# Performance work log

Measured on AMD Instinct MI355X. Metric: run time of the kernel, lower is better.

The kernel has to match this reference:

```python
import jax, jax.numpy as jnp
import numpy as np

S = 2048      # sequence length (q_seq == kv_seq, self-attention)
D = 1024      # hidden_size
H = 16        # num_heads
DH = D // H   # per-head dim
LN_EPS = 1e-5


def setup_inputs() -> dict:
    key = jax.random.key(0)
    ks = jax.random.split(key, 8)
    init = lambda k, shape: (jax.random.normal(k, shape, dtype=jnp.float32)
                             / np.float32(np.sqrt(shape[-1])))
    return {
        "x": jax.random.normal(ks[0], (S, D), dtype=jnp.float32),
        "logit_bias": jax.random.normal(ks[1], (S, H * S), dtype=jnp.float32) * 0.1,
        "mask": jax.random.bernoulli(ks[2], 0.9, (S, S)),
        "Wq": init(ks[3], (D, D)),
        "Wk": init(ks[4], (D, D)),
        "Wv": init(ks[5], (D, D)),
        "Wo": init(ks[6], (D, D)),
        "ln_w": jnp.ones((D,), dtype=jnp.float32),
        "ln_b": jnp.zeros((D,), dtype=jnp.float32),
    }


def reference(x, logit_bias, mask, Wq, Wk, Wv, Wo, ln_w, ln_b):
    # Projections (eqx.nn.Linear: y = W @ x, no bias), split into heads.
    q = (x @ Wq.T).reshape(S, H, DH)  # [s,h,d]
    k = (x @ Wk.T).reshape(S, H, DH)  # [S,h,d]
    v = (x @ Wv.T).reshape(S, H, DH)  # [S,h,d]

    # Scaled scores + per-head additive logit bias.
    scale = jnp.asarray(1.0 / np.sqrt(DH), dtype=q.dtype)
    logits = jnp.einsum('shd,Shd->hsS', q * scale, k)  # [h,s,S]
    logits = logits + logit_bias.reshape(S, H, S).transpose(1, 0, 2)

    # Boolean mask (q_seq, kv_seq) broadcast over heads.
    logits = jnp.where(mask[None, :, :], logits, jnp.finfo(logits.dtype).min)

    # Stable softmax in float32 (matches result_type promotion in source).
    weights = jax.nn.softmax(logits.astype(jnp.float32), axis=-1).astype(logits.dtype)

    attn = jnp.einsum('hsS,Shd->shd', weights, v).reshape(S, D)
    attn_out = attn @ Wo.T  # output projection, no bias

    # Residual + LayerNorm over last dim (eqx.nn.LayerNorm, eps=1e-5).
    res = attn_out + x
    mean = jnp.mean(res, axis=-1, keepdims=True)
    var = jnp.var(res, axis=-1, keepdims=True)
    normed = (res - mean) * jax.lax.rsqrt(var + LN_EPS)
    return normed * ln_w + ln_b
```

## Files before the change

kernel.cpp:

```cpp
#include <hip/hip_runtime.h>

#define SS 2048
#define DD 1024
#define HH 16
#define DHD 64
#define HSN (HH * SS)
#define LOG2E 1.44269504088896340736f

typedef __bf16 bf16x8 __attribute__((ext_vector_type(8)));
typedef __bf16 bf16x4 __attribute__((ext_vector_type(4)));
typedef float f32x4 __attribute__((ext_vector_type(4)));
typedef unsigned int u32;

__device__ __forceinline__ void glds16(const void* g, void* l) {
  __builtin_amdgcn_global_load_lds(
      (const __attribute__((address_space(1))) u32*)(const u32*)g,
      (__attribute__((address_space(3))) u32*)(u32*)l, 16, 0, 0);
}

__global__ __launch_bounds__(256) void cvt_all_kernel(const float* __restrict__ x,
                                                      const float* __restrict__ Wq,
                                                      const float* __restrict__ Wk,
                                                      const float* __restrict__ Wv,
                                                      const float* __restrict__ Wo,
                                                      __bf16* xb, __bf16* Wqb, __bf16* Wkb,
                                                      __bf16* Wvb, __bf16* Wob) {
  const int z = blockIdx.z;
  const int n4 = (z == 0 ? SS * DD : DD * DD) / 4;
  const int i = blockIdx.x * 256 + threadIdx.x;
  if (i >= n4) return;
  const float* in = z == 0 ? x : (z == 1 ? Wq : (z == 2 ? Wk : (z == 3 ? Wv : Wo)));
  __bf16* out = z == 0 ? xb : (z == 1 ? Wqb : (z == 2 ? Wkb : (z == 3 ? Wvb : Wob)));
  const float4 v = ((const float4*)in)[i];
  bf16x4 r;
  r[0] = (__bf16)v.x; r[1] = (__bf16)v.y; r[2] = (__bf16)v.z; r[3] = (__bf16)v.w;
  *(bf16x4*)&out[(long)i * 4] = r;
}

template <int OUTF32>
__device__ __forceinline__ void gemm128_body(const __bf16* __restrict__ A,
                                             const __bf16* __restrict__ B,
                                             void* __restrict__ Cout, float scale) {
  __shared__ alignas(16) __bf16 As[128 * 32];
  __shared__ alignas(16) __bf16 Bs[128 * 32];
  const int tid = threadIdx.x;
  const int lane = tid & 63;
  const int wave = tid >> 6;
  const long m0 = (long)blockIdx.y * 128;
  const long n0 = (long)blockIdx.x * 128;
  const int wm = (wave >> 1) * 64;
  const int wn = (wave & 1) * 64;
  const int g = lane >> 4, r16 = lane & 15;
  const int srow = tid >> 2, sseg = (tid & 3) * 8;

  f32x4 acc[4][4] = {};

  for (int k0 = 0; k0 < DD; k0 += 32) {
#pragma unroll
    for (int it = 0; it < 2; ++it) {
      const int row = srow + it * 64;
      glds16(&A[(m0 + row) * DD + k0 + sseg], &As[row * 32 + sseg]);
      glds16(&B[(n0 + row) * DD + k0 + sseg], &Bs[row * 32 + sseg]);
    }
    __syncthreads();
    bf16x8 af[4], bfr[4];
#pragma unroll
    for (int r = 0; r < 4; ++r) af[r] = *(const bf16x8*)&As[(wm + r * 16 + r16) * 32 + g * 8];
#pragma unroll
    for (int c = 0; c < 4; ++c) bfr[c] = *(const bf16x8*)&Bs[(wn + c * 16 + r16) * 32 + g * 8];
#pragma unroll
    for (int r = 0; r < 4; ++r)
#pragma unroll
      for (int c = 0; c < 4; ++c)
        acc[r][c] = __builtin_amdgcn_mfma_f32_16x16x32_bf16(af[r], bfr[c], acc[r][c], 0, 0, 0);
    __syncthreads();
  }

#pragma unroll
  for (int r = 0; r < 4; ++r)
#pragma unroll
    for (int c = 0; c < 4; ++c)
#pragma unroll
      for (int i = 0; i < 4; ++i) {
        const long row = m0 + wm + r * 16 + g * 4 + i;
        const long col = n0 + wn + c * 16 + r16;
        const float v = acc[r][c][i] * scale;
        if (OUTF32) ((float*)Cout)[row * DD + col] = v;
        else        ((__bf16*)Cout)[row * DD + col] = (__bf16)v;
      }
}

__global__ __launch_bounds__(256) void gemm_qkv(const __bf16* __restrict__ A,
                                                const __bf16* __restrict__ B0,
                                                const __bf16* __restrict__ B1,
                                                const __bf16* __restrict__ B2,
                                                __bf16* C0, __bf16* C1, __bf16* C2,
                                                float s0) {
  const __bf16* B = blockIdx.z == 0 ? B0 : (blockIdx.z == 1 ? B1 : B2);
  __bf16* C = blockIdx.z == 0 ? C0 : (blockIdx.z == 1 ? C1 : C2);
  gemm128_body<0>(A, B, C, blockIdx.z == 0 ? s0 : 1.0f);
}

__global__ __launch_bounds__(256) void gemm_o(const __bf16* __restrict__ A,
                                              const __bf16* __restrict__ B,
                                              float* __restrict__ C) {
  gemm128_body<1>(A, B, C, 1.0f);
}

__global__ __launch_bounds__(256) void transpose_bf16(const __bf16* __restrict__ in,
                                                      __bf16* __restrict__ out,
                                                      int R, int C) {
  __shared__ __bf16 t[64][72];
  const int tid = threadIdx.x;
  const long r0 = (long)blockIdx.y * 64;
  const long c0 = (long)blockIdx.x * 64;
  const int row = tid >> 2;
#pragma unroll
  for (int it = 0; it < 2; ++it) {
    const int seg = (tid & 3) * 8 + it * 32;
    *(bf16x8*)&t[row][seg] = *(const bf16x8*)&in[(r0 + row) * C + c0 + seg];
  }
  __syncthreads();
#pragma unroll
  for (int it = 0; it < 2; ++it) {
    const int seg = (tid & 3) * 8 + it * 32;
    bf16x8 v;
#pragma unroll
    for (int j = 0; j < 8; ++j) v[j] = t[seg + j][row];
    *(bf16x8*)&out[(c0 + row) * R + r0 + seg] = v;
  }
}

__global__ __launch_bounds__(256) void attn_kernel(
    const __bf16* __restrict__ Q, const __bf16* __restrict__ K,
    const __bf16* __restrict__ Vt, const float* __restrict__ bias,
    const int* __restrict__ mask, __bf16* __restrict__ Aout) {
  __shared__ alignas(16) __bf16 Ks[64][72];
  __shared__ alignas(16) __bf16 Vts[64][72];
  __shared__ alignas(16) __bf16 Ps[4][16][72];
  const int tid = threadIdx.x;
  const int lane = tid & 63;
  const int wave = tid >> 6;
  const int h = blockIdx.y;
  const int q0 = blockIdx.x * 64 + wave * 16;
  const int g = lane >> 4, r16 = lane & 15;
  const int myq = q0 + r16;

  bf16x8 qf[2];
#pragma unroll
  for (int c = 0; c < 2; ++c)
    qf[c] = *(const bf16x8*)&Q[(long)myq * DD + h * DHD + c * 32 + g * 8];

  f32x4 o[4] = {};
  float mrow = -__builtin_inff();
  float lsum = 0.f;

  const int srow = tid >> 2;

  for (int kv0 = 0; kv0 < SS; kv0 += 64) {
    __syncthreads();
#pragma unroll
    for (int it = 0; it < 2; ++it) {
      const int seg = (tid & 3) + it * 4;
      *(bf16x8*)&Ks[srow][seg * 8] =
          *(const bf16x8*)&K[(long)(kv0 + srow) * DD + h * DHD + seg * 8];
      *(bf16x8*)&Vts[srow][seg * 8] =
          *(const bf16x8*)&Vt[(long)(h * DHD + srow) * SS + kv0 + seg * 8];
    }

    float4 bv[4];
    int4 mv[4];
#pragma unroll
    for (int t = 0; t < 4; ++t) {
      const int kvi = kv0 + t * 16 + g * 4;
      bv[t] = *(const float4*)&bias[(long)myq * HSN + h * SS + kvi];
      mv[t] = *(const int4*)&mask[(long)myq * SS + kvi];
    }
    __syncthreads();

    f32x4 s[4];
#pragma unroll
    for (int t = 0; t < 4; ++t) {
      bf16x8 kf0 = *(const bf16x8*)&Ks[t * 16 + r16][g * 8];
      bf16x8 kf1 = *(const bf16x8*)&Ks[t * 16 + r16][32 + g * 8];
      f32x4 acc = {};
      acc = __builtin_amdgcn_mfma_f32_16x16x32_bf16(kf0, qf[0], acc, 0, 0, 0);
      s[t] = __builtin_amdgcn_mfma_f32_16x16x32_bf16(kf1, qf[1], acc, 0, 0, 0);
    }

    float sv[4][4];
#pragma unroll
    for (int t = 0; t < 4; ++t) {
      sv[t][0] = mv[t].x ? s[t][0] + bv[t].x * LOG2E : -1e38f;
      sv[t][1] = mv[t].y ? s[t][1] + bv[t].y * LOG2E : -1e38f;
      sv[t][2] = mv[t].z ? s[t][2] + bv[t].z * LOG2E : -1e38f;
      sv[t][3] = mv[t].w ? s[t][3] + bv[t].w * LOG2E : -1e38f;
    }

    float m4 = -1e38f;
#pragma unroll
    for (int t = 0; t < 4; ++t)
#pragma unroll
      for (int i = 0; i < 4; ++i) m4 = fmaxf(m4, sv[t][i]);
    m4 = fmaxf(m4, __shfl_xor(m4, 16));
    m4 = fmaxf(m4, __shfl_xor(m4, 32));
    const float mnew = fmaxf(mrow, m4);
    const float alpha = exp2f(mrow - mnew);
    float ps = 0.f;
    float p[4][4];
#pragma unroll
    for (int t = 0; t < 4; ++t)
#pragma unroll
      for (int i = 0; i < 4; ++i) {
        p[t][i] = exp2f(sv[t][i] - mnew);
        ps += p[t][i];
      }
    ps += __shfl_xor(ps, 16);
    ps += __shfl_xor(ps, 32);
    lsum = lsum * alpha + ps;
    mrow = mnew;
#pragma unroll
    for (int db = 0; db < 4; ++db) o[db] *= alpha;

#pragma unroll
    for (int t = 0; t < 4; ++t) {
      bf16x4 pb;
#pragma unroll
      for (int i = 0; i < 4; ++i) pb[i] = (__bf16)p[t][i];
      *(bf16x4*)&Ps[wave][r16][t * 16 + g * 4] = pb;
    }

#pragma unroll
    for (int kh = 0; kh < 2; ++kh) {
      bf16x8 pf = *(const bf16x8*)&Ps[wave][r16][kh * 32 + g * 8];
#pragma unroll
      for (int db = 0; db < 4; ++db) {
        bf16x8 vf = *(const bf16x8*)&Vts[db * 16 + r16][kh * 32 + g * 8];
        o[db] = __builtin_amdgcn_mfma_f32_16x16x32_bf16(vf, pf, o[db], 0, 0, 0);
      }
    }
  }

  const float rn = 1.f / lsum;
#pragma unroll
  for (int db = 0; db < 4; ++db) {
    bf16x4 r;
#pragma unroll
    for (int i = 0; i < 4; ++i) r[i] = (__bf16)(o[db][i] * rn);
    *(bf16x4*)&Aout[(long)myq * DD + h * DHD + db * 16 + g * 4] = r;
  }
}

__global__ __launch_bounds__(256) void ln_kernel(const float* __restrict__ attn_out,
                                                 const float* __restrict__ x,
                                                 const float* __restrict__ w,
                                                 const float* __restrict__ b,
                                                 float* __restrict__ out) {
  const long row = blockIdx.x;
  const int tid = threadIdx.x;
  float v[4];
  float s = 0.f, s2 = 0.f;
#pragma unroll
  for (int j = 0; j < 4; ++j) {
    const int d = tid + j * 256;
    const float r = attn_out[row * DD + d] + x[row * DD + d];
    v[j] = r; s += r; s2 += r * r;
  }
#pragma unroll
  for (int off = 1; off < 64; off <<= 1) {
    s  += __shfl_xor(s, off);
    s2 += __shfl_xor(s2, off);
  }
  __shared__ float ss[4], ss2[4];
  if ((tid & 63) == 0) { ss[tid >> 6] = s; ss2[tid >> 6] = s2; }
  __syncthreads();
  s = ss[0] + ss[1] + ss[2] + ss[3];
  s2 = ss2[0] + ss2[1] + ss2[2] + ss2[3];
  const float mean = s * (1.f / DD);
  const float var = s2 * (1.f / DD) - mean * mean;
  const float inv = rsqrtf(var + 1e-5f);
#pragma unroll
  for (int j = 0; j < 4; ++j) {
    const int d = tid + j * 256;
    out[row * DD + d] = (v[j] - mean) * inv * w[d] + b[d];
  }
}

extern "C" void kernel_launch(void* const* d_in, const int* in_sizes, int n_in,
                              void* d_out, int out_size, void* d_ws, size_t ws_size,
                              hipStream_t stream) {
  const float* x    = (const float*)d_in[0];
  const float* bias = (const float*)d_in[1];
  const int*   mask = (const int*)d_in[2];
  const float* Wq   = (const float*)d_in[3];
  const float* Wk   = (const float*)d_in[4];
  const float* Wv   = (const float*)d_in[5];
  const float* Wo   = (const float*)d_in[6];
  const float* lnw  = (const float*)d_in[7];
  const float* lnb  = (const float*)d_in[8];
  float* out = (float*)d_out;

  char* ws = (char*)d_ws;
  const size_t MB = 1024 * 1024;
  __bf16* xb   = (__bf16*)(ws + 0);
  __bf16* Wqb  = (__bf16*)(ws + 4 * MB);
  __bf16* Wkb  = (__bf16*)(ws + 6 * MB);
  __bf16* Wvb  = (__bf16*)(ws + 8 * MB);
  __bf16* Wob  = (__bf16*)(ws + 10 * MB);
  __bf16* Qb   = (__bf16*)(ws + 12 * MB);
  __bf16* Kb   = (__bf16*)(ws + 16 * MB);
  __bf16* Vb   = (__bf16*)(ws + 20 * MB);
  __bf16* Vtb  = (__bf16*)(ws + 24 * MB);
  __bf16* Atnb = (__bf16*)(ws + 28 * MB);
  float*  AOut = (float*)(ws + 32 * MB);

  cvt_all_kernel<<<dim3(SS * DD / 1024, 1, 5), dim3(256), 0, stream>>>(
      x, Wq, Wk, Wv, Wo, xb, Wqb, Wkb, Wvb, Wob);

  gemm_qkv<<<dim3(DD / 128, SS / 128, 3), dim3(256), 0, stream>>>(
      xb, Wqb, Wkb, Wvb, Qb, Kb, Vb, 0.125f * LOG2E);

  transpose_bf16<<<dim3(DD / 64, SS / 64), dim3(256), 0, stream>>>(Vb, Vtb, SS, DD);

  attn_kernel<<<dim3(SS / 64, HH), dim3(256), 0, stream>>>(Qb, Kb, Vtb, bias, mask, Atnb);

  gemm_o<<<dim3(DD / 128, SS / 128), dim3(256), 0, stream>>>(Atnb, Wob, AOut);

  ln_kernel<<<dim3(SS), dim3(256), 0, stream>>>(AOut, x, lnw, lnb, out);
}
```

Before: 492.9 us.

## Double-buffer GEMM LDS tiles and prefetch attention KV/bias/mask into registers

The GEMM body now uses two LDS buffers, so the next K-slice loads asynchronously while MFMAs run on the current one, and the per-step barrier count is halved. The output projection uses 64-row tiles to launch twice as many blocks. The attention kernel prefetches the next tile's K/V into registers and the next tile's bias and mask into ping-pong register sets before computing the current tile, so the dominant bias stream overlaps with compute. The cost is higher register and LDS pressure, plus a wasted wraparound prefetch on the last tile.

```diff
diff --git a/kernel.cpp b/kernel.cpp
--- a/kernel.cpp
+++ b/kernel.cpp
@@ -37,47 +37,61 @@
   *(bf16x4*)&out[(long)i * 4] = r;
 }
 
-template <int OUTF32>
-__device__ __forceinline__ void gemm128_body(const __bf16* __restrict__ A,
-                                             const __bf16* __restrict__ B,
-                                             void* __restrict__ Cout, float scale) {
-  __shared__ alignas(16) __bf16 As[128 * 32];
-  __shared__ alignas(16) __bf16 Bs[128 * 32];
+template <int BM, int OUTF32>
+__device__ __forceinline__ void gemm_body2(const __bf16* __restrict__ A,
+                                           const __bf16* __restrict__ B,
+                                           void* __restrict__ Cout, float scale) {
+  constexpr int MR = BM / 32;
+  __shared__ alignas(16) __bf16 As[2][BM * 32];
+  __shared__ alignas(16) __bf16 Bs[2][128 * 32];
   const int tid = threadIdx.x;
   const int lane = tid & 63;
   const int wave = tid >> 6;
-  const long m0 = (long)blockIdx.y * 128;
+  const long m0 = (long)blockIdx.y * BM;
   const long n0 = (long)blockIdx.x * 128;
-  const int wm = (wave >> 1) * 64;
+  const int wm = (wave >> 1) * (BM / 2);
   const int wn = (wave & 1) * 64;
   const int g = lane >> 4, r16 = lane & 15;
   const int srow = tid >> 2, sseg = (tid & 3) * 8;
 
-  f32x4 acc[4][4] = {};
-
-  for (int k0 = 0; k0 < DD; k0 += 32) {
+  f32x4 acc[MR][4] = {};
+
+  auto stage = [&](int buf, int k0) {
 #pragma unroll
     for (int it = 0; it < 2; ++it) {
       const int row = srow + it * 64;
-      glds16(&A[(m0 + row) * DD + k0 + sseg], &As[row * 32 + sseg]);
-      glds16(&B[(n0 + row) * DD + k0 + sseg], &Bs[row * 32 + sseg]);
-    }
-    __syncthreads();
-    bf16x8 af[4], bfr[4];
-#pragma unroll
-    for (int r = 0; r < 4; ++r) af[r] = *(const bf16x8*)&As[(wm + r * 16 + r16) * 32 + g * 8];
-#pragma unroll
-    for (int c = 0; c < 4; ++c) bfr[c] = *(const bf16x8*)&Bs[(wn + c * 16 + r16) * 32 + g * 8];
-#pragma unroll
-    for (int r = 0; r < 4; ++r)
+      glds16(&B[(n0 + row) * DD + k0 + sseg], &Bs[buf][row * 32 + sseg]);
+    }
+#pragma unroll
+    for (int it = 0; it < BM / 64; ++it) {
+      const int row = srow + it * 64;
+      glds16(&A[(m0 + row) * DD + k0 + sseg], &As[buf][row * 32 + sseg]);
+    }
+  };
+
+  stage(0, 0);
+  __syncthreads();
+  int cur = 0;
+  for (int kt = 0; kt < DD / 32; ++kt) {
+    if (kt + 1 < DD / 32) stage(cur ^ 1, (kt + 1) * 32);
+    bf16x8 af[MR], bfr[4];
+#pragma unroll
+    for (int r = 0; r < MR; ++r)
+      af[r] = *(const bf16x8*)&As[cur][(wm + r * 16 + r16) * 32 + g * 8];
+#pragma unroll
+    for (int c = 0; c < 4; ++c)
+      bfr[c] = *(const bf16x8*)&Bs[cur][(wn + c * 16 + r16) * 32 + g * 8];
+#pragma unroll
+    for (int r = 0; r < MR; ++r)
 #pragma unroll
       for (int c = 0; c < 4; ++c)
         acc[r][c] = __builtin_amdgcn_mfma_f32_16x16x32_bf16(af[r], bfr[c], acc[r][c], 0, 0, 0);
     __syncthreads();
-  }
-
-#pragma unroll
-  for (int r = 0; r < 4; ++r)
+    cur ^= 1;
+  }
+
+#pragma unroll
+  for (int r = 0; r < MR; ++r)
 #pragma unroll
     for (int c = 0; c < 4; ++c)
 #pragma unroll
@@ -98,13 +112,13 @@
                                                 float s0) {
   const __bf16* B = blockIdx.z == 0 ? B0 : (blockIdx.z == 1 ? B1 : B2);
   __bf16* C = blockIdx.z == 0 ? C0 : (blockIdx.z == 1 ? C1 : C2);
-  gemm128_body<0>(A, B, C, blockIdx.z == 0 ? s0 : 1.0f);
+  gemm_body2<128, 0>(A, B, C, blockIdx.z == 0 ? s0 : 1.0f);
 }
 
 __global__ __launch_bounds__(256) void gemm_o(const __bf16* __restrict__ A,
                                               const __bf16* __restrict__ B,
                                               float* __restrict__ C) {
-  gemm128_body<1>(A, B, C, 1.0f);
+  gemm_body2<64, 1>(A, B, C, 1.0f);
 }
 
 __global__ __launch_bounds__(256) void transpose_bf16(const __bf16* __restrict__ in,
@@ -128,6 +142,69 @@
 #pragma unroll
     for (int j = 0; j < 8; ++j) v[j] = t[seg + j][row];
     *(bf16x8*)&out[(c0 + row) * R + r0 + seg] = v;
+  }
+}
+
+__device__ __forceinline__ void attn_compute(
+    const float4 (&bv)[4], const int4 (&mv)[4], const bf16x8 (&qf)[2],
+    f32x4 (&o)[4], float& mrow, float& lsum,
+    __bf16 (*Ks)[72], __bf16 (*Vts)[72], __bf16 (*Psw)[72], int r16, int g) {
+  f32x4 s[4];
+#pragma unroll
+  for (int t = 0; t < 4; ++t) {
+    bf16x8 kf0 = *(const bf16x8*)&Ks[t * 16 + r16][g * 8];
+    bf16x8 kf1 = *(const bf16x8*)&Ks[t * 16 + r16][32 + g * 8];
+    f32x4 acc = {};
+    acc = __builtin_amdgcn_mfma_f32_16x16x32_bf16(kf0, qf[0], acc, 0, 0, 0);
+    s[t] = __builtin_amdgcn_mfma_f32_16x16x32_bf16(kf1, qf[1], acc, 0, 0, 0);
+  }
+  float sv[4][4];
+#pragma unroll
+  for (int t = 0; t < 4; ++t) {
+    sv[t][0] = mv[t].x ? s[t][0] + bv[t].x * LOG2E : -1e38f;
+    sv[t][1] = mv[t].y ? s[t][1] + bv[t].y * LOG2E : -1e38f;
+    sv[t][2] = mv[t].z ? s[t][2] + bv[t].z * LOG2E : -1e38f;
+    sv[t][3] = mv[t].w ? s[t][3] + bv[t].w * LOG2E : -1e38f;
+  }
+  float m4 = -1e38f;
+#pragma unroll
+  for (int t = 0; t < 4; ++t)
+#pragma unroll
+    for (int i = 0; i < 4; ++i) m4 = fmaxf(m4, sv[t][i]);
+  m4 = fmaxf(m4, __shfl_xor(m4, 16));
+  m4 = fmaxf(m4, __shfl_xor(m4, 32));
+  const float mnew = fmaxf(mrow, m4);
+  const float alpha = exp2f(mrow - mnew);
+  float ps = 0.f;
+  float p[4][4];
+#pragma unroll
+  for (int t = 0; t < 4; ++t)
+#pragma unroll
+    for (int i = 0; i < 4; ++i) {
+      p[t][i] = exp2f(sv[t][i] - mnew);
+      ps += p[t][i];
+    }
+  ps += __shfl_xor(ps, 16);
+  ps += __shfl_xor(ps, 32);
+  lsum = lsum * alpha + ps;
+  mrow = mnew;
+#pragma unroll
+  for (int db = 0; db < 4; ++db) o[db] *= alpha;
+#pragma unroll
+  for (int t = 0; t < 4; ++t) {
+    bf16x4 pb;
+#pragma unroll
+    for (int i = 0; i < 4; ++i) pb[i] = (__bf16)p[t][i];
+    *(bf16x4*)&Psw[r16][t * 16 + g * 4] = pb;
+  }
+#pragma unroll
+  for (int kh = 0; kh < 2; ++kh) {
+    bf16x8 pf = *(const bf16x8*)&Psw[r16][kh * 32 + g * 8];
+#pragma unroll
+    for (int db = 0; db < 4; ++db) {
+      bf16x8 vf = *(const bf16x8*)&Vts[db * 16 + r16][kh * 32 + g * 8];
+      o[db] = __builtin_amdgcn_mfma_f32_16x16x32_bf16(vf, pf, o[db], 0, 0, 0);
+    }
   }
 }
 
@@ -145,6 +222,7 @@
   const int q0 = blockIdx.x * 64 + wave * 16;
   const int g = lane >> 4, r16 = lane & 15;
   const int myq = q0 + r16;
+  const int srow = tid >> 2;
 
   bf16x8 qf[2];
 #pragma unroll
@@ -155,90 +233,47 @@
   float mrow = -__builtin_inff();
   float lsum = 0.f;
 
-  const int srow = tid >> 2;
-
-  for (int kv0 = 0; kv0 < SS; kv0 += 64) {
-    __syncthreads();
+  bf16x8 kreg[2], vreg[2];
+  float4 bvA[4], bvB[4];
+  int4 mvA[4], mvB[4];
+
+  auto loadKV = [&](int kv0) {
 #pragma unroll
     for (int it = 0; it < 2; ++it) {
       const int seg = (tid & 3) + it * 4;
-      *(bf16x8*)&Ks[srow][seg * 8] =
-          *(const bf16x8*)&K[(long)(kv0 + srow) * DD + h * DHD + seg * 8];
-      *(bf16x8*)&Vts[srow][seg * 8] =
-          *(const bf16x8*)&Vt[(long)(h * DHD + srow) * SS + kv0 + seg * 8];
-    }
-
-    float4 bv[4];
-    int4 mv[4];
+      kreg[it] = *(const bf16x8*)&K[(long)(kv0 + srow) * DD + h * DHD + seg * 8];
+      vreg[it] = *(const bf16x8*)&Vt[(long)(h * DHD + srow) * SS + kv0 + seg * 8];
+    }
+  };
+  auto loadBM = [&](int kv0, float4 (&bv)[4], int4 (&mv)[4]) {
 #pragma unroll
     for (int t = 0; t < 4; ++t) {
       const int kvi = kv0 + t * 16 + g * 4;
       bv[t] = *(const float4*)&bias[(long)myq * HSN + h * SS + kvi];
       mv[t] = *(const int4*)&mask[(long)myq * SS + kvi];
     }
+  };
+  auto tile = [&](int kvt, const float4 (&bvC)[4], const int4 (&mvC)[4],
+                  float4 (&bvN)[4], int4 (&mvN)[4]) {
     __syncthreads();
-
-    f32x4 s[4];
-#pragma unroll
-    for (int t = 0; t < 4; ++t) {
-      bf16x8 kf0 = *(const bf16x8*)&Ks[t * 16 + r16][g * 8];
-      bf16x8 kf1 = *(const bf16x8*)&Ks[t * 16 + r16][32 + g * 8];
-      f32x4 acc = {};
-      acc = __builtin_amdgcn_mfma_f32_16x16x32_bf16(kf0, qf[0], acc, 0, 0, 0);
-      s[t] = __builtin_amdgcn_mfma_f32_16x16x32_bf16(kf1, qf[1], acc, 0, 0, 0);
-    }
-
-    float sv[4][4];
-#pragma unroll
-    for (int t = 0; t < 4; ++t) {
-      sv[t][0] = mv[t].x ? s[t][0] + bv[t].x * LOG2E : -1e38f;
-      sv[t][1] = mv[t].y ? s[t][1] + bv[t].y * LOG2E : -1e38f;
-      sv[t][2] = mv[t].z ? s[t][2] + bv[t].z * LOG2E : -1e38f;
-      sv[t][3] = mv[t].w ? s[t][3] + bv[t].w * LOG2E : -1e38f;
-    }
-
-    float m4 = -1e38f;
-#pragma unroll
-    for (int t = 0; t < 4; ++t)
-#pragma unroll
-      for (int i = 0; i < 4; ++i) m4 = fmaxf(m4, sv[t][i]);
-    m4 = fmaxf(m4, __shfl_xor(m4, 16));
-    m4 = fmaxf(m4, __shfl_xor(m4, 32));
-    const float mnew = fmaxf(mrow, m4);
-    const float alpha = exp2f(mrow - mnew);
-    float ps = 0.f;
-    float p[4][4];
-#pragma unroll
-    for (int t = 0; t < 4; ++t)
-#pragma unroll
-      for (int i = 0; i < 4; ++i) {
-        p[t][i] = exp2f(sv[t][i] - mnew);
-        ps += p[t][i];
-      }
-    ps += __shfl_xor(ps, 16);
-    ps += __shfl_xor(ps, 32);
-    lsum = lsum * alpha + ps;
-    mrow = mnew;
-#pragma unroll
-    for (int db = 0; db < 4; ++db) o[db] *= alpha;
-
-#pragma unroll
-    for (int t = 0; t < 4; ++t) {
-      bf16x4 pb;
-#pragma unroll
-      for (int i = 0; i < 4; ++i) pb[i] = (__bf16)p[t][i];
-      *(bf16x4*)&Ps[wave][r16][t * 16 + g * 4] = pb;
-    }
-
-#pragma unroll
-    for (int kh = 0; kh < 2; ++kh) {
-      bf16x8 pf = *(const bf16x8*)&Ps[wave][r16][kh * 32 + g * 8];
-#pragma unroll
-      for (int db = 0; db < 4; ++db) {
-        bf16x8 vf = *(const bf16x8*)&Vts[db * 16 + r16][kh * 32 + g * 8];
-        o[db] = __builtin_amdgcn_mfma_f32_16x16x32_bf16(vf, pf, o[db], 0, 0, 0);
-      }
-    }
+#pragma unroll
+    for (int it = 0; it < 2; ++it) {
+      const int seg8 = ((tid & 3) + it * 4) * 8;
+      *(bf16x8*)&Ks[srow][seg8] = kreg[it];
+      *(bf16x8*)&Vts[srow][seg8] = vreg[it];
+    }
+    const int kvn = (kvt + 64 < SS) ? kvt + 64 : 0;
+    loadKV(kvn);
+    loadBM(kvn, bvN, mvN);
+    __syncthreads();
+    attn_compute(bvC, mvC, qf, o, mrow, lsum, Ks, Vts, Ps[wave], r16, g);
+  };
+
+  loadKV(0);
+  loadBM(0, bvA, mvA);
+  for (int kv0 = 0; kv0 < SS; kv0 += 128) {
+    tile(kv0, bvA, mvA, bvB, mvB);
+    tile(kv0 + 64, bvB, mvB, bvA, mvA);
   }
 
   const float rn = 1.f / lsum;
@@ -324,7 +359,7 @@
 
   attn_kernel<<<dim3(SS / 64, HH), dim3(256), 0, stream>>>(Qb, Kb, Vtb, bias, mask, Atnb);
 
-  gemm_o<<<dim3(DD / 128, SS / 128), dim3(256), 0, stream>>>(Atnb, Wob, AOut);
+  gemm_o<<<dim3(DD / 128, SS / 64), dim3(256), 0, stream>>>(Atnb, Wob, AOut);
 
   ln_kernel<<<dim3(SS), dim3(256), 0, stream>>>(AOut, x, lnw, lnb, out);
 }
```

Result: slower. 504.0 us (+2.3%).

## Pack mask to bits, fuse V transpose into QKV GEMM, retile output GEMM

Applied to the files above, without the earlier changes.

Adds a ballot-based kernel that packs the int mask into 64-bit words so the attention kernel reads one word per 64 keys instead of 64 ints, cutting mask traffic that was reread for every head. The V projection now writes its transposed layout directly from the GEMM epilogue, removing the separate transpose kernel and its round trip. The output projection uses a 64-row tile to launch more blocks. Risks are less coalesced transposed stores and an extra small launch.

```diff
diff --git a/kernel.cpp b/kernel.cpp
--- a/kernel.cpp
+++ b/kernel.cpp
@@ -11,6 +11,7 @@
 typedef __bf16 bf16x4 __attribute__((ext_vector_type(4)));
 typedef float f32x4 __attribute__((ext_vector_type(4)));
 typedef unsigned int u32;
+typedef unsigned long long u64;
 
 __device__ __forceinline__ void glds16(const void* g, void* l) {
   __builtin_amdgcn_global_load_lds(
@@ -37,57 +38,83 @@
   *(bf16x4*)&out[(long)i * 4] = r;
 }
 
-template <int OUTF32>
-__device__ __forceinline__ void gemm128_body(const __bf16* __restrict__ A,
-                                             const __bf16* __restrict__ B,
-                                             void* __restrict__ Cout, float scale) {
-  __shared__ alignas(16) __bf16 As[128 * 32];
+__global__ __launch_bounds__(256) void pack_mask(const int* __restrict__ mask,
+                                                 u64* __restrict__ mp) {
+  const long i = (long)blockIdx.x * 256 + threadIdx.x;
+  const u64 b = __ballot(mask[i] != 0);
+  if ((threadIdx.x & 63) == 0) mp[i >> 6] = b;
+}
+
+template <int BM>
+__device__ __forceinline__ void gemm_body(const __bf16* __restrict__ A,
+                                          const __bf16* __restrict__ B,
+                                          void* __restrict__ Cout, float scale, int mode) {
+  constexpr int MR = BM / 32;
+  __shared__ alignas(16) __bf16 As[BM * 32];
   __shared__ alignas(16) __bf16 Bs[128 * 32];
   const int tid = threadIdx.x;
   const int lane = tid & 63;
   const int wave = tid >> 6;
-  const long m0 = (long)blockIdx.y * 128;
+  const long m0 = (long)blockIdx.y * BM;
   const long n0 = (long)blockIdx.x * 128;
-  const int wm = (wave >> 1) * 64;
+  const int wm = (wave >> 1) * (BM / 2);
   const int wn = (wave & 1) * 64;
   const int g = lane >> 4, r16 = lane & 15;
   const int srow = tid >> 2, sseg = (tid & 3) * 8;
 
-  f32x4 acc[4][4] = {};
+  f32x4 acc[MR][4] = {};
 
   for (int k0 = 0; k0 < DD; k0 += 32) {
 #pragma unroll
     for (int it = 0; it < 2; ++it) {
       const int row = srow + it * 64;
+      glds16(&B[(n0 + row) * DD + k0 + sseg], &Bs[row * 32 + sseg]);
+    }
+#pragma unroll
+    for (int it = 0; it < BM / 64; ++it) {
+      const int row = srow + it * 64;
       glds16(&A[(m0 + row) * DD + k0 + sseg], &As[row * 32 + sseg]);
-      glds16(&B[(n0 + row) * DD + k0 + sseg], &Bs[row * 32 + sseg]);
     }
     __syncthreads();
-    bf16x8 af[4], bfr[4];
-#pragma unroll
-    for (int r = 0; r < 4; ++r) af[r] = *(const bf16x8*)&As[(wm + r * 16 + r16) * 32 + g * 8];
+    bf16x8 af[MR], bfr[4];
+#pragma unroll
+    for (int r = 0; r < MR; ++r) af[r] = *(const bf16x8*)&As[(wm + r * 16 + r16) * 32 + g * 8];
 #pragma unroll
     for (int c = 0; c < 4; ++c) bfr[c] = *(const bf16x8*)&Bs[(wn + c * 16 + r16) * 32 + g * 8];
 #pragma unroll
-    for (int r = 0; r < 4; ++r)
+    for (int r = 0; r < MR; ++r)
 #pragma unroll
       for (int c = 0; c < 4; ++c)
         acc[r][c] = __builtin_amdgcn_mfma_f32_16x16x32_bf16(af[r], bfr[c], acc[r][c], 0, 0, 0);
     __syncthreads();
   }
 
-#pragma unroll
-  for (int r = 0; r < 4; ++r)
-#pragma unroll
-    for (int c = 0; c < 4; ++c)
-#pragma unroll
-      for (int i = 0; i < 4; ++i) {
-        const long row = m0 + wm + r * 16 + g * 4 + i;
+  if (mode == 2) {
+#pragma unroll
+    for (int r = 0; r < MR; ++r)
+#pragma unroll
+      for (int c = 0; c < 4; ++c) {
+        const long row0 = m0 + wm + r * 16 + g * 4;
         const long col = n0 + wn + c * 16 + r16;
-        const float v = acc[r][c][i] * scale;
-        if (OUTF32) ((float*)Cout)[row * DD + col] = v;
-        else        ((__bf16*)Cout)[row * DD + col] = (__bf16)v;
+        bf16x4 rv;
+#pragma unroll
+        for (int i = 0; i < 4; ++i) rv[i] = (__bf16)(acc[r][c][i] * scale);
+        *(bf16x4*)&((__bf16*)Cout)[col * SS + row0] = rv;
       }
+  } else {
+#pragma unroll
+    for (int r = 0; r < MR; ++r)
+#pragma unroll
+      for (int c = 0; c < 4; ++c)
+#pragma unroll
+        for (int i = 0; i < 4; ++i) {
+          const long row = m0 + wm + r * 16 + g * 4 + i;
+          const long col = n0 + wn + c * 16 + r16;
+          const float v = acc[r][c][i] * scale;
+          if (mode == 1) ((float*)Cout)[row * DD + col] = v;
+          else           ((__bf16*)Cout)[row * DD + col] = (__bf16)v;
+        }
+  }
 }
 
 __global__ __launch_bounds__(256) void gemm_qkv(const __bf16* __restrict__ A,
@@ -96,45 +123,22 @@
                                                 const __bf16* __restrict__ B2,
                                                 __bf16* C0, __bf16* C1, __bf16* C2,
                                                 float s0) {
-  const __bf16* B = blockIdx.z == 0 ? B0 : (blockIdx.z == 1 ? B1 : B2);
-  __bf16* C = blockIdx.z == 0 ? C0 : (blockIdx.z == 1 ? C1 : C2);
-  gemm128_body<0>(A, B, C, blockIdx.z == 0 ? s0 : 1.0f);
+  const int z = blockIdx.z;
+  const __bf16* B = z == 0 ? B0 : (z == 1 ? B1 : B2);
+  __bf16* C = z == 0 ? C0 : (z == 1 ? C1 : C2);
+  gemm_body<128>(A, B, C, z == 0 ? s0 : 1.0f, z == 2 ? 2 : 0);
 }
 
 __global__ __launch_bounds__(256) void gemm_o(const __bf16* __restrict__ A,
                                               const __bf16* __restrict__ B,
                                               float* __restrict__ C) {
-  gemm128_body<1>(A, B, C, 1.0f);
-}
-
-__global__ __launch_bounds__(256) void transpose_bf16(const __bf16* __restrict__ in,
-                                                      __bf16* __restrict__ out,
-                                                      int R, int C) {
-  __shared__ __bf16 t[64][72];
-  const int tid = threadIdx.x;
-  const long r0 = (long)blockIdx.y * 64;
-  const long c0 = (long)blockIdx.x * 64;
-  const int row = tid >> 2;
-#pragma unroll
-  for (int it = 0; it < 2; ++it) {
-    const int seg = (tid & 3) * 8 + it * 32;
-    *(bf16x8*)&t[row][seg] = *(const bf16x8*)&in[(r0 + row) * C + c0 + seg];
-  }
-  __syncthreads();
-#pragma unroll
-  for (int it = 0; it < 2; ++it) {
-    const int seg = (tid & 3) * 8 + it * 32;
-    bf16x8 v;
-#pragma unroll
-    for (int j = 0; j < 8; ++j) v[j] = t[seg + j][row];
-    *(bf16x8*)&out[(c0 + row) * R + r0 + seg] = v;
-  }
+  gemm_body<64>(A, B, C, 1.0f, 1);
 }
 
 __global__ __launch_bounds__(256) void attn_kernel(
     const __bf16* __restrict__ Q, const __bf16* __restrict__ K,
     const __bf16* __restrict__ Vt, const float* __restrict__ bias,
-    const int* __restrict__ mask, __bf16* __restrict__ Aout) {
+    const u64* __restrict__ mp, __bf16* __restrict__ Aout) {
   __shared__ alignas(16) __bf16 Ks[64][72];
   __shared__ alignas(16) __bf16 Vts[64][72];
   __shared__ alignas(16) __bf16 Ps[4][16][72];
@@ -145,17 +149,19 @@
   const int q0 = blockIdx.x * 64 + wave * 16;
   const int g = lane >> 4, r16 = lane & 15;
   const int myq = q0 + r16;
+  const int srow = tid >> 2;
 
   bf16x8 qf[2];
 #pragma unroll
   for (int c = 0; c < 2; ++c)
     qf[c] = *(const bf16x8*)&Q[(long)myq * DD + h * DHD + c * 32 + g * 8];
+
+  const float* bp = &bias[(long)myq * HSN + h * SS];
+  const u64* mrow_p = &mp[(long)myq * (SS / 64)];
 
   f32x4 o[4] = {};
   float mrow = -__builtin_inff();
   float lsum = 0.f;
-
-  const int srow = tid >> 2;
 
   for (int kv0 = 0; kv0 < SS; kv0 += 64) {
     __syncthreads();
@@ -169,13 +175,9 @@
     }
 
     float4 bv[4];
-    int4 mv[4];
-#pragma unroll
-    for (int t = 0; t < 4; ++t) {
-      const int kvi = kv0 + t * 16 + g * 4;
-      bv[t] = *(const float4*)&bias[(long)myq * HSN + h * SS + kvi];
-      mv[t] = *(const int4*)&mask[(long)myq * SS + kvi];
-    }
+#pragma unroll
+    for (int t = 0; t < 4; ++t) bv[t] = *(const float4*)&bp[kv0 + t * 16 + g * 4];
+    const u64 mw = mrow_p[kv0 >> 6];
     __syncthreads();
 
     f32x4 s[4];
@@ -191,10 +193,11 @@
     float sv[4][4];
 #pragma unroll
     for (int t = 0; t < 4; ++t) {
-      sv[t][0] = mv[t].x ? s[t][0] + bv[t].x * LOG2E : -1e38f;
-      sv[t][1] = mv[t].y ? s[t][1] + bv[t].y * LOG2E : -1e38f;
-      sv[t][2] = mv[t].z ? s[t][2] + bv[t].z * LOG2E : -1e38f;
-      sv[t][3] = mv[t].w ? s[t][3] + bv[t].w * LOG2E : -1e38f;
+      const u32 mb = (u32)(mw >> (t * 16 + g * 4));
+      sv[t][0] = (mb & 1u) ? s[t][0] + bv[t].x * LOG2E : -1e38f;
+      sv[t][1] = (mb & 2u) ? s[t][1] + bv[t].y * LOG2E : -1e38f;
+      sv[t][2] = (mb & 4u) ? s[t][2] + bv[t].z * LOG2E : -1e38f;
+      sv[t][3] = (mb & 8u) ? s[t][3] + bv[t].w * LOG2E : -1e38f;
     }
 
     float m4 = -1e38f;
@@ -309,22 +312,22 @@
   __bf16* Wob  = (__bf16*)(ws + 10 * MB);
   __bf16* Qb   = (__bf16*)(ws + 12 * MB);
   __bf16* Kb   = (__bf16*)(ws + 16 * MB);
-  __bf16* Vb   = (__bf16*)(ws + 20 * MB);
   __bf16* Vtb  = (__bf16*)(ws + 24 * MB);
   __bf16* Atnb = (__bf16*)(ws + 28 * MB);
   float*  AOut = (float*)(ws + 32 * MB);
+  u64*    mpk  = (u64*)(ws + 40 * MB);
 
   cvt_all_kernel<<<dim3(SS * DD / 1024, 1, 5), dim3(256), 0, stream>>>(
       x, Wq, Wk, Wv, Wo, xb, Wqb, Wkb, Wvb, Wob);
 
+  pack_mask<<<dim3(SS * SS / 256), dim3(256), 0, stream>>>(mask, mpk);
+
   gemm_qkv<<<dim3(DD / 128, SS / 128, 3), dim3(256), 0, stream>>>(
-      xb, Wqb, Wkb, Wvb, Qb, Kb, Vb, 0.125f * LOG2E);
-
-  transpose_bf16<<<dim3(DD / 64, SS / 64), dim3(256), 0, stream>>>(Vb, Vtb, SS, DD);
-
-  attn_kernel<<<dim3(SS / 64, HH), dim3(256), 0, stream>>>(Qb, Kb, Vtb, bias, mask, Atnb);
-
-  gemm_o<<<dim3(DD / 128, SS / 128), dim3(256), 0, stream>>>(Atnb, Wob, AOut);
+      xb, Wqb, Wkb, Wvb, Qb, Kb, Vtb, 0.125f * LOG2E);
+
+  attn_kernel<<<dim3(SS / 64, HH), dim3(256), 0, stream>>>(Qb, Kb, Vtb, bias, mpk, Atnb);
+
+  gemm_o<<<dim3(DD / 128, SS / 64), dim3(256), 0, stream>>>(Atnb, Wob, AOut);
 
   ln_kernel<<<dim3(SS), dim3(256), 0, stream>>>(AOut, x, lnw, lnb, out);
 }
```

Measured after the change: 488.0 us. About the same (-1.0%).
